# Optimization experiments

Hardware: AMD Instinct MI355X
Metric: run time of the kernel (lower is better)

The kernel has to match this reference:

```python
import jax, jax.numpy as jnp
import numpy as np

NUM_EXPERTS = 8
IN_FEATURES = 1024
HIDDEN_FEATURES = 4096
OUT_FEATURES = 1024
TOKENS = 8192


def setup_inputs() -> dict:
    key = jax.random.key(0)
    k_x, k_idx, k_w1, k_w2, k_b1, k_b2 = jax.random.split(key, 6)
    x = jax.random.normal(k_x, (TOKENS, IN_FEATURES), dtype=jnp.float32)
    indices_s = jax.random.randint(k_idx, (TOKENS,), 0, NUM_EXPERTS, dtype=jnp.int64)
    # learned parameters (torch uses torch.rand; scaled for numeric sanity)
    weight1 = jax.random.normal(k_w1, (NUM_EXPERTS, IN_FEATURES, HIDDEN_FEATURES), dtype=jnp.float32) * 0.02
    weight2 = jax.random.normal(k_w2, (NUM_EXPERTS, HIDDEN_FEATURES, OUT_FEATURES), dtype=jnp.float32) * 0.02
    bias1 = jax.random.normal(k_b1, (NUM_EXPERTS, HIDDEN_FEATURES), dtype=jnp.float32) * 0.02
    bias2 = jax.random.normal(k_b2, (NUM_EXPERTS, IN_FEATURES), dtype=jnp.float32) * 0.02
    return {"x": x, "indices_s": indices_s, "weight1": weight1, "weight2": weight2, "bias1": bias1, "bias2": bias2}


def reference(x, indices_s, weight1, weight2, bias1, bias2):
    # Per-token expert MLP. Rather than gathering full weight matrices per
    # token (weight[indices_s] -> [T, in, hid], huge), loop over the small
    # fixed expert set and mask-combine. Math identical to the torch module.
    T = x.shape[0]
    num_experts = weight1.shape[0]
    out = jnp.zeros((T, weight2.shape[2]), dtype=x.dtype)
    for e in range(num_experts):
        mask = (indices_s == e)[:, None]  # [T, 1]
        h = jax.nn.gelu(x @ weight1[e] + bias1[e], approximate=False)  # [T, hid]
        y = h @ weight2[e] + bias2[e]  # [T, out]
        out = out + jnp.where(mask, y, jnp.zeros((), dtype=x.dtype))
    # original returns shape [T, 1, out] (x was unsqueezed)
    return out[:, None, :]
```

## Files before the change

### kernel.cpp

```cpp
#include <hip/hip_runtime.h>
#include <hip/hip_bf16.h>
#include <math.h>

#define TOKENS 8192
#define IN_F   1024
#define HID_F  4096
#define OUT_F  1024
#define NEXP   8
#define TSLOTS 40

typedef __attribute__((ext_vector_type(8))) short bf16x8;
typedef __attribute__((ext_vector_type(4))) float f32x4;
typedef __attribute__((ext_vector_type(8))) unsigned short u16x8;

__device__ __forceinline__ unsigned short f2bf(float f) {
    unsigned int u = __float_as_uint(f);
    u += 0x7fffu + ((u >> 16) & 1u);
    return (unsigned short)(u >> 16);
}

__device__ __forceinline__ void gload_lds16(const unsigned short* g, unsigned char* lds) {
    __builtin_amdgcn_global_load_lds(
        (const __attribute__((address_space(1))) void*)g,
        (__attribute__((address_space(3))) void*)lds, 16, 0, 0);
}

__global__ void sort_kernel(const int* __restrict__ idx, int* __restrict__ perm,
                            int* __restrict__ off, int* __restrict__ table) {
    __shared__ int cnt[NEXP];
    __shared__ int base[NEXP];
    const int tid = threadIdx.x, lane = tid & 63;
    if (tid < NEXP) cnt[tid] = 0;
    __syncthreads();
    for (int i = tid; i < TOKENS; i += 1024) {
        int e = idx[i];
#pragma unroll
        for (int ex = 0; ex < NEXP; ++ex) {
            unsigned long long m = __ballot(e == ex);
            if (lane == 0 && m) atomicAdd(&cnt[ex], __popcll(m));
        }
    }
    __syncthreads();
    if (tid == 0) {
        int s = 0;
        for (int e = 0; e < NEXP; ++e) { off[e] = s; base[e] = s; s += cnt[e]; }
        off[NEXP] = s;
        int t = 0;
        for (int e = 0; e < NEXP; ++e)
            for (int m0 = off[e]; m0 < off[e + 1]; m0 += 256)
                table[t++] = (e << 13) | m0;
        for (; t < TSLOTS; ++t) table[t] = -1;
    }
    __syncthreads();
    for (int i = tid; i < TOKENS; i += 1024) {
        int e = idx[i];
#pragma unroll
        for (int ex = 0; ex < NEXP; ++ex) {
            unsigned long long m = __ballot(e == ex);
            if (e == ex) {
                int lead = (int)__ffsll((long long)m) - 1;
                int pos = 0;
                if (lane == lead) pos = atomicAdd(&base[ex], __popcll(m));
                pos = __shfl(pos, lead);
                pos += __popcll(m & ((1ULL << lane) - 1ULL));
                perm[pos] = i;
            }
        }
    }
}

__global__ void gather_x(const float* __restrict__ x, const int* __restrict__ perm,
                         unsigned short* __restrict__ xg) {
    const int row = blockIdx.x, t = threadIdx.x;
    const int src = perm[row];
    float4 v = *(const float4*)(x + (size_t)src * IN_F + t * 4);
    unsigned long long pk =
        (unsigned long long)f2bf(v.x) |
        ((unsigned long long)f2bf(v.y) << 16) |
        ((unsigned long long)f2bf(v.z) << 32) |
        ((unsigned long long)f2bf(v.w) << 48);
    *(unsigned long long*)(xg + (size_t)row * IN_F + t * 4) = pk;
}

__global__ void transp(const float* __restrict__ in, unsigned short* __restrict__ out,
                       int R, int C) {
    __shared__ unsigned short T[64 * 65];
    const int e = blockIdx.z;
    const int r0 = blockIdx.y * 64, c0 = blockIdx.x * 64;
    const int tid = threadIdx.x;
    const int rr = tid >> 4, cc = tid & 15;
    const float* ip = in + ((size_t)e * R + r0) * C + c0;
#pragma unroll
    for (int p = 0; p < 4; ++p) {
        int r = p * 16 + rr;
        float4 v = *(const float4*)(ip + (size_t)r * C + cc * 4);
        T[(cc * 4 + 0) * 65 + r] = f2bf(v.x);
        T[(cc * 4 + 1) * 65 + r] = f2bf(v.y);
        T[(cc * 4 + 2) * 65 + r] = f2bf(v.z);
        T[(cc * 4 + 3) * 65 + r] = f2bf(v.w);
    }
    __syncthreads();
    unsigned short* op = out + ((size_t)e * C + c0) * R + r0;
    const int c = tid >> 2, ch = tid & 3;
    u16x8 a, b;
#pragma unroll
    for (int i = 0; i < 8; ++i) a[i] = T[c * 65 + ch * 16 + i];
#pragma unroll
    for (int i = 0; i < 8; ++i) b[i] = T[c * 65 + ch * 16 + 8 + i];
    *(u16x8*)(op + (size_t)c * R + ch * 16) = a;
    *(u16x8*)(op + (size_t)c * R + ch * 16 + 8) = b;
}

template<int K, int ND, bool GELU>
__launch_bounds__(512, 2)
__global__ void moe_gemm256(const unsigned short* __restrict__ A,
                            const unsigned short* __restrict__ W,
                            const float* __restrict__ bias,
                            const int* __restrict__ perm,
                            const int* __restrict__ off,
                            const int* __restrict__ table,
                            void* __restrict__ outp) {
    const int nwg = (ND / 256) * TSLOTS;
    const int chunk = nwg >> 3;
    const int logical = ((int)blockIdx.x & 7) * chunk + ((int)blockIdx.x >> 3);
    const int nt = logical / TSLOTS;
    const int t0 = logical - nt * TSLOTS;
    const int te = table[t0];
    if (te < 0) return;
    const int e  = te >> 13;
    const int m0 = te & 8191;
    const int sege = off[e + 1];
    const int n0 = nt * 256;

    __shared__ __align__(16) unsigned char L[131072];

    const int tid = threadIdx.x;
    const int wid = tid >> 6, lane = tid & 63;
    const int wr = wid >> 2, wc = wid & 3;
    const int lr = lane & 15, hk = lane >> 4;

    const unsigned short* We = W + (size_t)e * ND * K + (size_t)n0 * K;

    const int srow8 = lane >> 3;
    const int sch   = (lane & 7) ^ srow8;
    const unsigned short* aSrc[4];
    const unsigned short* wSrc[4];
#pragma unroll
    for (int cc = 0; cc < 4; ++cc) {
        int rt = cc * 64 + wid * 8 + srow8;
        int ga = m0 + rt; if (ga > TOKENS - 1) ga = TOKENS - 1;
        aSrc[cc] = A  + (size_t)ga * K + sch * 8;
        wSrc[cc] = We + (size_t)rt * K + sch * 8;
    }
    const int dstBase = wid * 1024;

    constexpr int NT = K / 64;

    auto stageH = [&](int tile, int h) {
        const int buf = (tile & 1) * 65536;
        const int op  = (h >> 1) * 32768;
        const int c0_ = (h & 1) * 2;
        const int ko  = tile * 64;
#pragma unroll
        for (int j = 0; j < 2; ++j) {
            int cc = c0_ + j;
            const unsigned short* s = (h < 2) ? (aSrc[cc] + ko) : (wSrc[cc] + ko);
            gload_lds16(s, L + buf + op + cc * 8192 + dstBase);
        }
    };

    f32x4 acc[8][4];
#pragma unroll
    for (int i = 0; i < 8; ++i)
#pragma unroll
        for (int j = 0; j < 4; ++j) acc[i][j] = (f32x4){0.f, 0.f, 0.f, 0.f};

#pragma unroll
    for (int h = 0; h < 4; ++h) stageH(0, h);

    const int xorc = (lr & 7) << 4;

    for (int t = 0; t < NT; ++t) {
        __builtin_amdgcn_s_barrier();
        if (t + 1 < NT) {
            stageH(t + 1, 0);
            asm volatile("s_waitcnt vmcnt(2)" ::: "memory");
        } else {
            asm volatile("s_waitcnt vmcnt(0)" ::: "memory");
        }
        __builtin_amdgcn_s_barrier();
        __builtin_amdgcn_sched_barrier(0);

        const unsigned char* rb = L + (t & 1) * 65536;

        bf16x8 b[4][2];
#pragma unroll
        for (int n = 0; n < 4; ++n) {
            int row = wc * 64 + n * 16 + lr;
#pragma unroll
            for (int kk = 0; kk < 2; ++kk)
                b[n][kk] = *(const bf16x8*)(rb + 32768 + row * 128 + ((((kk * 4 + hk) << 4) ^ xorc)));
        }

        bf16x8 a[4][2];
#pragma unroll
        for (int m = 0; m < 4; ++m) {
            int row = wr * 128 + m * 16 + lr;
#pragma unroll
            for (int kk = 0; kk < 2; ++kk)
                a[m][kk] = *(const bf16x8*)(rb + row * 128 + ((((kk * 4 + hk) << 4) ^ xorc)));
        }
        if (t + 1 < NT) stageH(t + 1, 1);
        __builtin_amdgcn_s_setprio(1);
#pragma unroll
        for (int m = 0; m < 4; ++m)
#pragma unroll
            for (int n = 0; n < 4; ++n)
#pragma unroll
                for (int kk = 0; kk < 2; ++kk)
                    acc[m][n] = __builtin_amdgcn_mfma_f32_16x16x32_bf16(a[m][kk], b[n][kk], acc[m][n], 0, 0, 0);
        __builtin_amdgcn_s_setprio(0);

#pragma unroll
        for (int m = 0; m < 4; ++m) {
            int row = wr * 128 + 64 + m * 16 + lr;
#pragma unroll
            for (int kk = 0; kk < 2; ++kk)
                a[m][kk] = *(const bf16x8*)(rb + row * 128 + ((((kk * 4 + hk) << 4) ^ xorc)));
        }
        if (t + 1 < NT) stageH(t + 1, 2);
        __builtin_amdgcn_s_setprio(1);
#pragma unroll
        for (int m = 0; m < 4; ++m)
#pragma unroll
            for (int n = 0; n < 4; ++n)
#pragma unroll
                for (int kk = 0; kk < 2; ++kk)
                    acc[4 + m][n] = __builtin_amdgcn_mfma_f32_16x16x32_bf16(a[m][kk], b[n][kk], acc[4 + m][n], 0, 0, 0);
        __builtin_amdgcn_s_setprio(0);
        if (t + 1 < NT) stageH(t + 1, 3);
    }

    const float* be = bias + (size_t)e * ND + n0;
#pragma unroll
    for (int m = 0; m < 8; ++m) {
#pragma unroll
        for (int r = 0; r < 4; ++r) {
            int row = wr * 128 + m * 16 + hk * 4 + r;
            int grow = m0 + row;
            if (grow >= sege) continue;
            if constexpr (GELU) {
                unsigned short* h = (unsigned short*)outp;
                size_t base = (size_t)grow * ND + n0;
#pragma unroll
                for (int n = 0; n < 4; ++n) {
                    int col = wc * 64 + n * 16 + lr;
                    float v = acc[m][n][r] + be[col];
                    float u = v * (0.7978845608f + 0.0356774081f * v * v);
                    float g = v / (1.0f + __expf(-2.0f * u));
                    h[base + col] = f2bf(g);
                }
            } else {
                float* out = (float*)outp;
                int tok = perm[grow];
                size_t base = (size_t)tok * ND + n0;
#pragma unroll
                for (int n = 0; n < 4; ++n) {
                    int col = wc * 64 + n * 16 + lr;
                    out[base + col] = acc[m][n][r] + be[col];
                }
            }
        }
    }
}

extern "C" void kernel_launch(void* const* d_in, const int* in_sizes, int n_in,
                              void* d_out, int out_size, void* d_ws, size_t ws_size,
                              hipStream_t stream) {
    const float* x   = (const float*)d_in[0];
    const int*   idx = (const int*)d_in[1];
    const float* w1  = (const float*)d_in[2];
    const float* w2  = (const float*)d_in[3];
    const float* b1  = (const float*)d_in[4];
    const float* b2  = (const float*)d_in[5];
    float* out = (float*)d_out;

    int* perm  = (int*)d_ws;
    int* off   = perm + TOKENS;
    int* table = off + 16;
    unsigned short* xg = (unsigned short*)((char*)d_ws + 65536);
    unsigned short* h  = xg + (size_t)TOKENS * IN_F;
    unsigned short* wt = h + (size_t)TOKENS * HID_F;

    hipLaunchKernelGGL(sort_kernel, dim3(1), dim3(1024), 0, stream, idx, perm, off, table);
    hipLaunchKernelGGL(gather_x, dim3(TOKENS), dim3(256), 0, stream, x, perm, xg);

    hipLaunchKernelGGL(transp, dim3(HID_F / 64, IN_F / 64, NEXP), dim3(256), 0, stream,
                       w1, wt, IN_F, HID_F);
    hipLaunchKernelGGL((moe_gemm256<IN_F, HID_F, true>), dim3((HID_F / 256) * TSLOTS), dim3(512),
                       0, stream, xg, wt, b1, perm, off, table, (void*)h);

    hipLaunchKernelGGL(transp, dim3(OUT_F / 64, HID_F / 64, NEXP), dim3(256), 0, stream,
                       w2, wt, HID_F, OUT_F);
    hipLaunchKernelGGL((moe_gemm256<HID_F, OUT_F, false>), dim3((OUT_F / 256) * TSLOTS), dim3(512),
                       0, stream, h, wt, b2, perm, off, table, (void*)out);
}
```

Measured before the change: 341.7 us.

## Restructure GEMM main loop into 8-phase ping-pong schedule with split B reads

```diff
diff --git a/kernel.cpp b/kernel.cpp
--- a/kernel.cpp
+++ b/kernel.cpp
@@ -111,21 +111,42 @@
     *(u16x8*)(op + (size_t)c * R + ch * 16 + 8) = b;
 }
 
+#define RD_A(RB, HALF) \
+  _Pragma("unroll") for (int m_ = 0; m_ < 4; ++m_) { \
+    const int row_ = wr * 128 + (HALF) * 64 + m_ * 16 + lr; \
+    _Pragma("unroll") for (int kk_ = 0; kk_ < 2; ++kk_) \
+      aR[m_][kk_] = *(const bf16x8*)((RB) + row_ * 128 + (((kk_ * 4 + hk) << 4) ^ xorc)); }
+
+#define RD_B(RB, NH, DST) \
+  _Pragma("unroll") for (int nn_ = 0; nn_ < 2; ++nn_) { \
+    const int row_ = wc * 64 + ((NH) * 2 + nn_) * 16 + lr; \
+    _Pragma("unroll") for (int kk_ = 0; kk_ < 2; ++kk_) \
+      DST[nn_][kk_] = *(const bf16x8*)((RB) + 32768 + row_ * 128 + (((kk_ * 4 + hk) << 4) ^ xorc)); }
+
+#define MFMA_Q(MH, NH, B) \
+  __builtin_amdgcn_s_setprio(1); \
+  _Pragma("unroll") for (int m_ = 0; m_ < 4; ++m_) \
+    _Pragma("unroll") for (int nn_ = 0; nn_ < 2; ++nn_) \
+      _Pragma("unroll") for (int kk_ = 0; kk_ < 2; ++kk_) \
+        acc[(MH) * 4 + m_][(NH) * 2 + nn_] = __builtin_amdgcn_mfma_f32_16x16x32_bf16( \
+            aR[m_][kk_], B[nn_][kk_], acc[(MH) * 4 + m_][(NH) * 2 + nn_], 0, 0, 0); \
+  __builtin_amdgcn_s_setprio(0);
+
 template<int K, int ND, bool GELU>
 __launch_bounds__(512, 2)
-__global__ void moe_gemm256(const unsigned short* __restrict__ A,
-                            const unsigned short* __restrict__ W,
-                            const float* __restrict__ bias,
-                            const int* __restrict__ perm,
-                            const int* __restrict__ off,
-                            const int* __restrict__ table,
-                            void* __restrict__ outp) {
+__global__ void moe_gemm8p(const unsigned short* __restrict__ A,
+                           const unsigned short* __restrict__ W,
+                           const float* __restrict__ bias,
+                           const int* __restrict__ perm,
+                           const int* __restrict__ off,
+                           const int* __restrict__ table,
+                           void* __restrict__ outp) {
     const int nwg = (ND / 256) * TSLOTS;
     const int chunk = nwg >> 3;
     const int logical = ((int)blockIdx.x & 7) * chunk + ((int)blockIdx.x >> 3);
     const int nt = logical / TSLOTS;
-    const int t0 = logical - nt * TSLOTS;
-    const int te = table[t0];
+    const int ts = logical - nt * TSLOTS;
+    const int te = table[ts];
     if (te < 0) return;
     const int e  = te >> 13;
     const int m0 = te & 8191;
@@ -175,70 +196,66 @@
 #pragma unroll
         for (int j = 0; j < 4; ++j) acc[i][j] = (f32x4){0.f, 0.f, 0.f, 0.f};
 
-#pragma unroll
-    for (int h = 0; h < 4; ++h) stageH(0, h);
-
+    bf16x8 aR[4][2], b0R[2][2], b1R[2][2];
     const int xorc = (lr & 7) << 4;
-
-    for (int t = 0; t < NT; ++t) {
-        __builtin_amdgcn_s_barrier();
-        if (t + 1 < NT) {
-            stageH(t + 1, 0);
-            asm volatile("s_waitcnt vmcnt(2)" ::: "memory");
-        } else {
-            asm volatile("s_waitcnt vmcnt(0)" ::: "memory");
-        }
+    const unsigned char* rb0 = L;
+    const unsigned char* rb1 = L + 65536;
+
+    stageH(0, 0); stageH(0, 1); stageH(0, 2); stageH(0, 3);
+    stageH(1, 0);
+    asm volatile("s_waitcnt vmcnt(2)" ::: "memory");
+    __builtin_amdgcn_s_barrier();
+    __builtin_amdgcn_sched_barrier(0);
+
+#pragma unroll 1
+    for (int i = 0; i < NT / 2; ++i) {
+        const int T1 = 2 * i + 1;
+        const bool lastIt = (i == NT / 2 - 1);
+        RD_A(rb0, 0); RD_B(rb0, 0, b0R);
+        stageH(T1, 1);
+        __builtin_amdgcn_s_barrier();
+        MFMA_Q(0, 0, b0R);
+        __builtin_amdgcn_s_barrier();
+        RD_B(rb0, 1, b1R);
+        stageH(T1, 2);
+        __builtin_amdgcn_s_barrier();
+        MFMA_Q(0, 1, b1R);
+        __builtin_amdgcn_s_barrier();
+        RD_A(rb0, 1);
+        stageH(T1, 3);
+        __builtin_amdgcn_s_barrier();
+        MFMA_Q(1, 1, b1R);
+        __builtin_amdgcn_s_barrier();
+        RD_B(rb0, 0, b0R);
+        if (!lastIt) stageH(T1 + 1, 0);
+        __builtin_amdgcn_s_barrier();
+        MFMA_Q(1, 0, b0R);
+        if (lastIt) { asm volatile("s_waitcnt vmcnt(0)" ::: "memory"); }
+        else        { asm volatile("s_waitcnt vmcnt(2)" ::: "memory"); }
         __builtin_amdgcn_s_barrier();
         __builtin_amdgcn_sched_barrier(0);
-
-        const unsigned char* rb = L + (t & 1) * 65536;
-
-        bf16x8 b[4][2];
-#pragma unroll
-        for (int n = 0; n < 4; ++n) {
-            int row = wc * 64 + n * 16 + lr;
-#pragma unroll
-            for (int kk = 0; kk < 2; ++kk)
-                b[n][kk] = *(const bf16x8*)(rb + 32768 + row * 128 + ((((kk * 4 + hk) << 4) ^ xorc)));
-        }
-
-        bf16x8 a[4][2];
-#pragma unroll
-        for (int m = 0; m < 4; ++m) {
-            int row = wr * 128 + m * 16 + lr;
-#pragma unroll
-            for (int kk = 0; kk < 2; ++kk)
-                a[m][kk] = *(const bf16x8*)(rb + row * 128 + ((((kk * 4 + hk) << 4) ^ xorc)));
-        }
-        if (t + 1 < NT) stageH(t + 1, 1);
-        __builtin_amdgcn_s_setprio(1);
-#pragma unroll
-        for (int m = 0; m < 4; ++m)
-#pragma unroll
-            for (int n = 0; n < 4; ++n)
-#pragma unroll
-                for (int kk = 0; kk < 2; ++kk)
-                    acc[m][n] = __builtin_amdgcn_mfma_f32_16x16x32_bf16(a[m][kk], b[n][kk], acc[m][n], 0, 0, 0);
-        __builtin_amdgcn_s_setprio(0);
-
-#pragma unroll
-        for (int m = 0; m < 4; ++m) {
-            int row = wr * 128 + 64 + m * 16 + lr;
-#pragma unroll
-            for (int kk = 0; kk < 2; ++kk)
-                a[m][kk] = *(const bf16x8*)(rb + row * 128 + ((((kk * 4 + hk) << 4) ^ xorc)));
-        }
-        if (t + 1 < NT) stageH(t + 1, 2);
-        __builtin_amdgcn_s_setprio(1);
-#pragma unroll
-        for (int m = 0; m < 4; ++m)
-#pragma unroll
-            for (int n = 0; n < 4; ++n)
-#pragma unroll
-                for (int kk = 0; kk < 2; ++kk)
-                    acc[4 + m][n] = __builtin_amdgcn_mfma_f32_16x16x32_bf16(a[m][kk], b[n][kk], acc[4 + m][n], 0, 0, 0);
-        __builtin_amdgcn_s_setprio(0);
-        if (t + 1 < NT) stageH(t + 1, 3);
+        RD_A(rb1, 0); RD_B(rb1, 0, b0R);
+        if (!lastIt) stageH(T1 + 1, 1);
+        __builtin_amdgcn_s_barrier();
+        MFMA_Q(0, 0, b0R);
+        __builtin_amdgcn_s_barrier();
+        RD_B(rb1, 1, b1R);
+        if (!lastIt) stageH(T1 + 1, 2);
+        __builtin_amdgcn_s_barrier();
+        MFMA_Q(0, 1, b1R);
+        __builtin_amdgcn_s_barrier();
+        RD_A(rb1, 1);
+        if (!lastIt) stageH(T1 + 1, 3);
+        __builtin_amdgcn_s_barrier();
+        MFMA_Q(1, 1, b1R);
+        __builtin_amdgcn_s_barrier();
+        RD_B(rb1, 0, b0R);
+        if (!lastIt) stageH(T1 + 2, 0);
+        __builtin_amdgcn_s_barrier();
+        MFMA_Q(1, 0, b0R);
+        if (!lastIt) { asm volatile("s_waitcnt vmcnt(2)" ::: "memory"); }
+        __builtin_amdgcn_s_barrier();
+        __builtin_amdgcn_sched_barrier(0);
     }
 
     const float* be = bias + (size_t)e * ND + n0;
@@ -297,11 +314,11 @@
 
     hipLaunchKernelGGL(transp, dim3(HID_F / 64, IN_F / 64, NEXP), dim3(256), 0, stream,
                        w1, wt, IN_F, HID_F);
-    hipLaunchKernelGGL((moe_gemm256<IN_F, HID_F, true>), dim3((HID_F / 256) * TSLOTS), dim3(512),
+    hipLaunchKernelGGL((moe_gemm8p<IN_F, HID_F, true>), dim3((HID_F / 256) * TSLOTS), dim3(512),
                        0, stream, xg, wt, b1, perm, off, table, (void*)h);
 
     hipLaunchKernelGGL(transp, dim3(OUT_F / 64, HID_F / 64, NEXP), dim3(256), 0, stream,
                        w2, wt, HID_F, OUT_F);
-    hipLaunchKernelGGL((moe_gemm256<HID_F, OUT_F, false>), dim3((OUT_F / 256) * TSLOTS), dim3(512),
+    hipLaunchKernelGGL((moe_gemm8p<HID_F, OUT_F, false>), dim3((OUT_F / 256) * TSLOTS), dim3(512),
                        0, stream, h, wt, b2, perm, off, table, (void*)out);
 }
```

After: 338.0 us. About the same (-1.1%).
